# Optimization experiments

Hardware: AMD Instinct MI355X
Metric: run time of the kernel (lower is better)

The kernel has to match this reference:

```python
import jax, jax.numpy as jnp
import numpy as np

V, H, KS, VS, T, N, L = 8000, 512, 128, 128, 500, 64, 200


def setup_inputs() -> dict:
    k = jax.random.key(0)
    ks = jax.random.split(k, 16)
    s = 0.05
    emb = jax.random.normal(ks[0], (V, H), jnp.float32) * s
    emb = emb.at[0].set(0.0)  # padding_idx=0
    return {
        "key": jax.random.normal(ks[1], (T, N, KS), jnp.float32),
        "values": jax.random.normal(ks[2], (T, N, VS), jnp.float32),
        "lens": jax.random.randint(ks[3], (N,), 1, T + 1, jnp.int32),
        "text": jax.random.randint(ks[4], (N, L), 1, V, jnp.int32),
        "emb": emb,
        "W_ih1": jax.random.normal(ks[5], (4 * H, H + VS), jnp.float32) * s,
        "W_hh1": jax.random.normal(ks[6], (4 * H, H), jnp.float32) * s,
        "b_ih1": jax.random.normal(ks[7], (4 * H,), jnp.float32) * s,
        "b_hh1": jax.random.normal(ks[8], (4 * H,), jnp.float32) * s,
        "W_ih2": jax.random.normal(ks[9], (4 * KS, H), jnp.float32) * s,
        "W_hh2": jax.random.normal(ks[10], (4 * KS, KS), jnp.float32) * s,
        "b_ih2": jax.random.normal(ks[11], (4 * KS,), jnp.float32) * s,
        "b_hh2": jax.random.normal(ks[12], (4 * KS,), jnp.float32) * s,
        "W_out": jax.random.normal(ks[13], (V, KS + VS), jnp.float32) * s,
        "b_out": jax.random.normal(ks[14], (V,), jnp.float32) * s,
    }


def _lstm_cell(x, h, c, Wih, Whh, bih, bhh):
    # PyTorch LSTMCell: gates in order i, f, g, o
    z = x @ Wih.T + bih + h @ Whh.T + bhh
    i, f, g, o = jnp.split(z, 4, axis=-1)
    c2 = jax.nn.sigmoid(f) * c + jax.nn.sigmoid(i) * jnp.tanh(g)
    h2 = jax.nn.sigmoid(o) * jnp.tanh(c2)
    return h2, c2


def reference(key, values, lens, text, emb, W_ih1, W_hh1, b_ih1, b_hh1,
              W_ih2, W_hh2, b_ih2, b_hh2, W_out, b_out):
    dt = values.dtype
    # teacher-forced embeddings for all steps; padding_idx=0 -> zero vec, no grad
    embeds = emb[text] * (text != 0).astype(dt)[..., None]      # (N, L, H)
    embeds_t = jnp.swapaxes(embeds, 0, 1)                        # (L, N, H)
    key_nt = jnp.swapaxes(key, 0, 1)                             # (N, T, KS)
    val_nt = jnp.swapaxes(values, 0, 1)                          # (N, T, VS)
    pad_mask = jnp.arange(key.shape[0])[None, :] >= lens[:, None]  # (N, T)

    n = key.shape[1]
    h1 = jnp.zeros((n, W_hh1.shape[1]), dt)
    c1 = jnp.zeros_like(h1)
    h2 = jnp.zeros((n, W_hh2.shape[1]), dt)
    c2 = jnp.zeros_like(h2)
    ctx0 = values[0]  # step 0 uses values[0]; later steps use attention context

    def step(carry, char_embed):
        h1, c1, h2, c2, ctx = carry
        inp = jnp.concatenate([char_embed, ctx], axis=1)
        h1, c1 = _lstm_cell(inp, h1, c1, W_ih1, W_hh1, b_ih1, b_hh1)
        h2, c2 = _lstm_cell(h1, h2, c2, W_ih2, W_hh2, b_ih2, b_hh2)
        # attention: query = h2
        energy = jnp.einsum("ntk,nk->nt", key_nt, h2)
        energy = jnp.where(pad_mask, jnp.asarray(-1e9, dt), energy)
        attn = jax.nn.softmax(energy, axis=1)
        ctx = jnp.einsum("nt,ntv->nv", attn, val_nt)
        pred = jnp.concatenate([h2, ctx], axis=1) @ W_out.T + b_out
        return (h1, c1, h2, c2, ctx), pred

    _, preds = jax.lax.scan(step, (h1, c1, h2, c2, ctx0), embeds_t)
    return jnp.swapaxes(preds, 0, 1)  # (N, L, V)
```

## Files before the change

kernel.cpp:

```cpp
#include <hip/hip_runtime.h>
#include <hip/hip_bf16.h>


typedef __bf16 bf16;
typedef __attribute__((ext_vector_type(8))) __bf16 bf16x8;
typedef __attribute__((ext_vector_type(4))) float f32x4;
typedef unsigned int uint;

#define MFMA(a, b, c) __builtin_amdgcn_mfma_f32_16x16x32_bf16((a), (b), (c), 0, 0, 0)

#define O_X1     0UL
#define O_EMBB   52428800UL
#define O_C1     52428800UL
#define O_C2     52559872UL
#define O_WEMBP  60620800UL
#define O_WZ1    62717952UL
#define O_WZ2    65339392UL
#define O_B1P    65994752UL
#define O_B2P    66002944UL
#define O_WOUTB  66004992UL
#define O_KEYB   70100992UL
#define O_VALB   78292992UL
#define O_H1     86484992UL
#define O_H2     86616064UL
#define O_PART   86648832UL
#define O_H2CTX  86718464UL

#define AA_WA   0
#define AA_CTX  20736
#define AA_ZS   29440
#define A_LDS   46336

#define BB_WB   0
#define BB_ZS   41472
#define B_LDS   58368

#define CC_KEY  0
#define CC_VAL  33000
#define CC_EL   66000
#define CC_PL   66512
#define CC_H2F  67024
#define CC_RED  67536
#define C_LDS   67600

__device__ inline float sigf(float x) { return 1.f / (1.f + __expf(-x)); }
__device__ inline float tanhf_(float x) { float e = __expf(2.f * x); return 1.f - 2.f / (e + 1.f); }
__device__ inline float bflo(uint u) { union { uint u; float f; } c; c.u = u << 16; return c.f; }
__device__ inline float bfhi(uint u) { union { uint u; float f; } c; c.u = u & 0xffff0000u; return c.f; }
__device__ inline float wred_max(float v) {
#pragma unroll
  for (int m = 32; m; m >>= 1) v = fmaxf(v, __shfl_xor(v, m, 64));
  return v;
}
__device__ inline float wred_sum(float v) {
#pragma unroll
  for (int m = 32; m; m >>= 1) v += __shfl_xor(v, m, 64);
  return v;
}

__global__ __launch_bounds__(256) void prep_kernel(
    const float* __restrict__ key, const float* __restrict__ values,
    const float* __restrict__ emb, const float* __restrict__ Wih1,
    const float* __restrict__ Whh1, const float* __restrict__ bih1,
    const float* __restrict__ bhh1, const float* __restrict__ Wih2,
    const float* __restrict__ Whh2, const float* __restrict__ bih2,
    const float* __restrict__ bhh2, const float* __restrict__ Wout,
    char* __restrict__ ws) {
  long g = (long)blockIdx.x * 256 + threadIdx.x;
  long str = (long)gridDim.x * 256;
  bf16* embB = (bf16*)(ws + O_EMBB);
  bf16* WembP = (bf16*)(ws + O_WEMBP);
  bf16* Wz1p = (bf16*)(ws + O_WZ1);
  bf16* Wz2p = (bf16*)(ws + O_WZ2);
  float* b1p = (float*)(ws + O_B1P);
  float* b2p = (float*)(ws + O_B2P);
  bf16* WoutB = (bf16*)(ws + O_WOUTB);
  bf16* keyB = (bf16*)(ws + O_KEYB);
  bf16* valB = (bf16*)(ws + O_VALB);

  for (long i = g; i < 8000L * 512; i += str) embB[i] = (bf16)emb[i];
  for (long i = g; i < 2048L * 512; i += str) {
    long gg = i >> 9, k = i & 511;
    long pg = (gg & 3) * 512 + (gg >> 2);
    WembP[i] = (bf16)Wih1[pg * 640 + k];
  }
  for (long i = g; i < 2048L * 640; i += str) {
    long gg = i / 640, k = i - gg * 640;
    long pg = (gg & 3) * 512 + (gg >> 2);
    float v = (k < 128) ? Wih1[pg * 640 + 512 + k] : Whh1[pg * 512 + (k - 128)];
    Wz1p[i] = (bf16)v;
  }
  for (long i = g; i < 512L * 640; i += str) {
    long gg = i / 640, k = i - gg * 640;
    long pg = (gg & 3) * 128 + (gg >> 2);
    float v = (k < 128) ? Whh2[pg * 128 + k] : Wih2[pg * 512 + (k - 128)];
    Wz2p[i] = (bf16)v;
  }
  for (long i = g; i < 2048; i += str) {
    long pg = (i & 3) * 512 + (i >> 2);
    b1p[i] = bih1[pg] + bhh1[pg];
  }
  for (long i = g; i < 512; i += str) {
    long pg = (i & 3) * 128 + (i >> 2);
    b2p[i] = bih2[pg] + bhh2[pg];
  }
  for (long i = g; i < 8000L * 256; i += str) WoutB[i] = (bf16)Wout[i];
  for (long i = g; i < 500L * 64 * 128; i += str) {
    keyB[i] = (bf16)key[i];
    valB[i] = (bf16)values[i];
  }
  uint* z = (uint*)(ws + O_H1);
  for (long i = g; i < 40960; i += str) z[i] = 0u;
}

__global__ __launch_bounds__(256) void k1_gemm(const int* __restrict__ text,
                                               char* __restrict__ ws) {
  const int tid = threadIdx.x, lane = tid & 63, wave = tid >> 6;
  const int l15 = lane & 15, quad = lane >> 4;
  const int Nb = blockIdx.x, Mb = blockIdx.y;
  const bf16* embB = (const bf16*)(ws + O_EMBB);
  const bf16* WembP = (const bf16*)(ws + O_WEMBP);
  const float* b1p = (const float*)(ws + O_B1P);
  bf16* X1 = (bf16*)(ws + O_X1);

  int m = Mb * 64 + wave * 16 + l15;
  int tcol = m >> 6, n = m & 63;
  int vid = text[n * 200 + tcol];
  const bf16* arow = embB + (size_t)vid * 512 + quad * 8;

  f32x4 acc[4];
#pragma unroll
  for (int nt = 0; nt < 4; ++nt) {
    float b = b1p[Nb * 64 + nt * 16 + l15];
    acc[nt] = (f32x4){b, b, b, b};
  }
  for (int kt = 0; kt < 16; ++kt) {
    bf16x8 af = *(const bf16x8*)(arow + kt * 32);
#pragma unroll
    for (int nt = 0; nt < 4; ++nt) {
      bf16x8 bfr = *(const bf16x8*)(WembP + (size_t)(Nb * 64 + nt * 16 + l15) * 512 +
                                    kt * 32 + quad * 8);
      acc[nt] = MFMA(af, bfr, acc[nt]);
    }
  }
#pragma unroll
  for (int nt = 0; nt < 4; ++nt)
#pragma unroll
    for (int r = 0; r < 4; ++r) {
      int mr = Mb * 64 + wave * 16 + quad * 4 + r;
      X1[(size_t)mr * 2048 + Nb * 64 + nt * 16 + l15] = (bf16)acc[nt][r];
    }
}

__device__ inline void combine_ctx(int t, int nA0, int ga, int tid,
                                   bf16* __restrict__ ctx_base, const char* __restrict__ part,
                                   bf16* __restrict__ h2ctx, bool wlds) {
  int m = tid >> 3, kk = tid & 7;
  const char* pb = part + (size_t)(nA0 + m) * 4 * 272;
  float mc0 = ((const float*)(pb))[0], sc0 = ((const float*)(pb))[1];
  float mc1 = ((const float*)(pb + 272))[0], sc1 = ((const float*)(pb + 272))[1];
  float mc2 = ((const float*)(pb + 544))[0], sc2 = ((const float*)(pb + 544))[1];
  float mc3 = ((const float*)(pb + 816))[0], sc3 = ((const float*)(pb + 816))[1];
  float M = fmaxf(fmaxf(mc0, mc1), fmaxf(mc2, mc3));
  float w0 = __expf(mc0 - M), w1 = __expf(mc1 - M);
  float w2 = __expf(mc2 - M), w3 = __expf(mc3 - M);
  float S = sc0 * w0 + sc1 * w1 + sc2 * w2 + sc3 * w3;
  float inv = 1.f / S;
  const bf16* x0 = (const bf16*)(pb + 8);
  const bf16* x1 = (const bf16*)(pb + 280);
  const bf16* x2 = (const bf16*)(pb + 552);
  const bf16* x3 = (const bf16*)(pb + 824);
#pragma unroll
  for (int i = 0; i < 16; ++i) {
    int k = kk * 16 + i;
    float v = w0 * (float)x0[k] + w1 * (float)x1[k] + w2 * (float)x2[k] + w3 * (float)x3[k];
    bf16 hv = (bf16)(v * inv);
    if (wlds) ctx_base[m * 136 + k] = hv;
    if (ga == 0) h2ctx[(size_t)((t - 1) * 64 + nA0 + m) * 256 + 128 + k] = hv;
  }
}

__global__ __launch_bounds__(256) void phaseA(const float* __restrict__ values,
                                              int t, char* __restrict__ ws) {
  extern __shared__ __align__(16) char smem[];
  const int bid = blockIdx.x, tid = threadIdx.x;
  const int lane = tid & 63, wave = tid >> 6;
  const int l15 = lane & 15, quad = lane >> 4;
  const int ra = bid & 1, ga = bid >> 1;
  const int nA0 = 32 * ra;
  const int p = t & 1;

  const bf16* Wz1p = (const bf16*)(ws + O_WZ1);
  const bf16* X1 = (const bf16*)(ws + O_X1);
  bf16* h1b = (bf16*)(ws + O_H1);
  char* part = ws + O_PART;
  bf16* h2ctx = (bf16*)(ws + O_H2CTX);
  float* c1g = (float*)(ws + O_C1);

  for (int i = tid; i < 16 * 80; i += 256) {
    int r = i / 80, c = i % 80;
    *(uint4*)(smem + AA_WA + r * 1296 + c * 16) =
        *(const uint4*)((const char*)Wz1p + (size_t)(16 * ga + r) * 1280 + c * 16);
  }
  if (t == 0) {
    int m = tid >> 3, kk = tid & 7;
    bf16* ctxL = (bf16*)(smem + AA_CTX) + m * 136;
#pragma unroll
    for (int i = 0; i < 16; ++i) {
      int k = kk * 16 + i;
      ctxL[k] = (bf16)values[(nA0 + m) * 128 + k];
    }
  } else {
    combine_ctx(t, nA0, ga, tid, (bf16*)(smem + AA_CTX), part, h2ctx, true);
  }
  __syncthreads();
  {
    f32x4 acc0 = {0, 0, 0, 0}, acc1 = {0, 0, 0, 0};
    const bf16* h1p = h1b + p * 32768;
#pragma unroll
    for (int q = 0; q < 5; ++q) {
      int kt = wave * 5 + q;
      bf16x8 bfr = *(const bf16x8*)(smem + AA_WA + l15 * 1296 + (kt * 32 + quad * 8) * 2);
      bf16x8 a0, a1;
      if (kt < 4) {
        a0 = *(const bf16x8*)(smem + AA_CTX + l15 * 272 + (kt * 32 + quad * 8) * 2);
        a1 = *(const bf16x8*)(smem + AA_CTX + (16 + l15) * 272 + (kt * 32 + quad * 8) * 2);
      } else {
        const bf16* base = h1p + (kt - 4) * 32 + quad * 8;
        a0 = *(const bf16x8*)(base + (size_t)(nA0 + l15) * 512);
        a1 = *(const bf16x8*)(base + (size_t)(nA0 + 16 + l15) * 512);
      }
      acc0 = MFMA(a0, bfr, acc0);
      acc1 = MFMA(a1, bfr, acc1);
    }
    float* zs = (float*)(smem + AA_ZS) + wave * 1056;
#pragma unroll
    for (int r = 0; r < 4; ++r) {
      zs[(quad * 4 + r) * 33 + l15] = acc0[r];
      zs[(16 + quad * 4 + r) * 33 + l15] = acc1[r];
    }
  }
  __syncthreads();
  if (tid < 128) {
    int m = tid >> 2, j = tid & 3;
    float zi = 0, zf = 0, zg = 0, zo = 0;
    const float* zr = (const float*)(smem + AA_ZS);
#pragma unroll
    for (int w = 0; w < 4; ++w) {
      const float* q_ = zr + w * 1056 + m * 33 + 4 * j;
      zi += q_[0]; zf += q_[1]; zg += q_[2]; zo += q_[3];
    }
    const bf16* xp = X1 + (size_t)(t * 64 + nA0 + m) * 2048 + ga * 16 + 4 * j;
    zi += (float)xp[0]; zf += (float)xp[1]; zg += (float)xp[2]; zo += (float)xp[3];
    int ci = (nA0 + m) * 512 + ga * 4 + j;
    float cprev = (t == 0) ? 0.f : c1g[ci];
    float c = sigf(zf) * cprev + sigf(zi) * tanhf_(zg);
    float h = sigf(zo) * tanhf_(c);
    c1g[ci] = c;
    h1b[(p ^ 1) * 32768 + (size_t)(nA0 + m) * 512 + ga * 4 + j] = (bf16)h;
  }
}

__global__ __launch_bounds__(256) void phaseB(int t, char* __restrict__ ws) {
  extern __shared__ __align__(16) char smem[];
  const int bid = blockIdx.x, tid = threadIdx.x;
  const int lane = tid & 63, wave = tid >> 6;
  const int l15 = lane & 15, quad = lane >> 4;
  const int hb = bid >> 1;
  const int nB0 = 32 * (bid & 1);
  const int p = t & 1;

  const bf16* Wz2p = (const bf16*)(ws + O_WZ2);
  const float* b2p = (const float*)(ws + O_B2P);
  bf16* h1b = (bf16*)(ws + O_H1);
  bf16* h2b = (bf16*)(ws + O_H2);
  bf16* h2ctx = (bf16*)(ws + O_H2CTX);
  float* c2g = (float*)(ws + O_C2);

  for (int i = tid; i < 32 * 80; i += 256) {
    int r = i / 80, c = i % 80;
    *(uint4*)(smem + BB_WB + r * 1296 + c * 16) =
        *(const uint4*)((const char*)Wz2p + (size_t)(32 * hb + r) * 1280 + c * 16);
  }
  __syncthreads();
  {
    f32x4 a00 = {0, 0, 0, 0}, a01 = {0, 0, 0, 0}, a10 = {0, 0, 0, 0}, a11 = {0, 0, 0, 0};
    const bf16* h2p = h2b + p * 8192;
    const bf16* h1n = h1b + (p ^ 1) * 32768;
#pragma unroll
    for (int q = 0; q < 5; ++q) {
      int kt = wave * 5 + q;
      bf16x8 b0 = *(const bf16x8*)(smem + BB_WB + l15 * 1296 + (kt * 32 + quad * 8) * 2);
      bf16x8 b1 = *(const bf16x8*)(smem + BB_WB + (16 + l15) * 1296 + (kt * 32 + quad * 8) * 2);
      bf16x8 a0, a1;
      if (kt < 4) {
        const bf16* base = h2p + kt * 32 + quad * 8;
        a0 = *(const bf16x8*)(base + (size_t)(nB0 + l15) * 128);
        a1 = *(const bf16x8*)(base + (size_t)(nB0 + 16 + l15) * 128);
      } else {
        const bf16* base = h1n + (kt - 4) * 32 + quad * 8;
        a0 = *(const bf16x8*)(base + (size_t)(nB0 + l15) * 512);
        a1 = *(const bf16x8*)(base + (size_t)(nB0 + 16 + l15) * 512);
      }
      a00 = MFMA(a0, b0, a00); a01 = MFMA(a0, b1, a01);
      a10 = MFMA(a1, b0, a10); a11 = MFMA(a1, b1, a11);
    }
    float* zs = (float*)(smem + BB_ZS) + wave * 1056;
#pragma unroll
    for (int r = 0; r < 4; ++r) {
      zs[(quad * 4 + r) * 33 + l15] = a00[r];
      zs[(quad * 4 + r) * 33 + 16 + l15] = a01[r];
      zs[(16 + quad * 4 + r) * 33 + l15] = a10[r];
      zs[(16 + quad * 4 + r) * 33 + 16 + l15] = a11[r];
    }
  }
  __syncthreads();
  {
    int m = tid >> 3, jj = tid & 7;
    float zi = 0, zf = 0, zg = 0, zo = 0;
    const float* zr = (const float*)(smem + BB_ZS);
#pragma unroll
    for (int w = 0; w < 4; ++w) {
      const float* q_ = zr + w * 1056 + m * 33 + 4 * jj;
      zi += q_[0]; zf += q_[1]; zg += q_[2]; zo += q_[3];
    }
    const float* bb = b2p + 32 * hb + 4 * jj;
    zi += bb[0]; zf += bb[1]; zg += bb[2]; zo += bb[3];
    int ci = (nB0 + m) * 128 + 8 * hb + jj;
    float cprev = (t == 0) ? 0.f : c2g[ci];
    float c = sigf(zf) * cprev + sigf(zi) * tanhf_(zg);
    float h = sigf(zo) * tanhf_(c);
    c2g[ci] = c;
    bf16 hv = (bf16)h;
    h2b[(p ^ 1) * 8192 + (size_t)(nB0 + m) * 128 + 8 * hb + jj] = hv;
    h2ctx[(size_t)(t * 64 + nB0 + m) * 256 + 8 * hb + jj] = hv;
  }
}

__global__ __launch_bounds__(256) void phaseC(const int* __restrict__ lens,
                                              int t, char* __restrict__ ws) {
  extern __shared__ __align__(16) char smem[];
  const int bid = blockIdx.x, tid = threadIdx.x;
  const int lane = tid & 63, w = tid >> 6;
  const int nc = bid >> 2, cc = bid & 3;
  const int p = t & 1;

  const bf16* keyB = (const bf16*)(ws + O_KEYB);
  const bf16* valB = (const bf16*)(ws + O_VALB);
  const bf16* h2b = (const bf16*)(ws + O_H2);
  char* part = ws + O_PART;

  float* eL = (float*)(smem + CC_EL);
  float* pL = (float*)(smem + CC_PL);
  float* h2f = (float*)(smem + CC_H2F);
  float* red = (float*)(smem + CC_RED);

  for (int i = tid; i < 125 * 32; i += 256) {
    int r = i >> 5, c = i & 31;
    size_t src = ((size_t)(cc * 125 + r) * 64 + nc) * 256 + c * 8;
    *(uint2*)(smem + CC_KEY + r * 264 + c * 8) = *(const uint2*)((const char*)keyB + src);
    *(uint2*)(smem + CC_VAL + r * 264 + c * 8) = *(const uint2*)((const char*)valB + src);
  }
  if (tid < 128) h2f[tid] = (float)h2b[(p ^ 1) * 8192 + (size_t)nc * 128 + tid];
  const int lenr = lens[nc];
  __syncthreads();

  if (tid < 125) {
    int gt = cc * 125 + tid;
    float e = -1e30f;
    if (gt < lenr) {
      const uint* kr = (const uint*)(smem + CC_KEY + tid * 264);
      float s = 0.f;
#pragma unroll 8
      for (int k2 = 0; k2 < 64; ++k2) {
        uint u = kr[k2];
        s += h2f[2 * k2] * bflo(u) + h2f[2 * k2 + 1] * bfhi(u);
      }
      e = s;
    }
    eL[tid] = e;
  } else if (tid < 128) {
    eL[tid] = -1e30f;
  }
  __syncthreads();
  if (tid < 64) {
    float v = fmaxf(eL[tid], eL[tid + 64]);
    v = wred_max(v);
    if (tid == 0) red[0] = v;
  }
  __syncthreads();
  float mC = red[0];
  if (tid < 128) {
    float pv = 0.f;
    if (tid < 125 && (cc * 125 + tid) < lenr) pv = __expf(eL[tid] - mC);
    pL[tid] = pv;
  }
  __syncthreads();
  if (tid < 64) {
    float v = pL[tid] + pL[tid + 64];
    v = wred_sum(v);
    if (tid == 0) red[1] = v;
  }
  __syncthreads();
  {
    char* pbase = part + (size_t)(nc * 4 + cc) * 272;
    if (tid == 0) {
      ((float*)pbase)[0] = mC;
      ((float*)pbase)[1] = red[1];
    }
    if (tid < 64) {
      const char* vbase = smem + CC_VAL + tid * 4;
      float a0 = 0.f, a1 = 0.f;
      for (int tt = 0; tt < 125; ++tt) {
        float pv = pL[tt];
        uint u = *(const uint*)(vbase + tt * 264);
        a0 += pv * bflo(u);
        a1 += pv * bfhi(u);
      }
      bf16* dst = (bf16*)(pbase + 8);
      dst[2 * tid] = (bf16)a0;
      dst[2 * tid + 1] = (bf16)a1;
    }
  }
}

__global__ __launch_bounds__(256) void ctx_final(char* __restrict__ ws) {
  const int nA0 = 32 * blockIdx.x, tid = threadIdx.x;
  combine_ctx(200, nA0, 0, tid, nullptr, ws + O_PART, (bf16*)(ws + O_H2CTX), false);
}

__global__ __launch_bounds__(256) void k4_gemm(const float* __restrict__ bout,
                                               float* __restrict__ out,
                                               char* __restrict__ ws) {
  const int tid = threadIdx.x, lane = tid & 63, wave = tid >> 6;
  const int l15 = lane & 15, quad = lane >> 4;
  const int Nb = blockIdx.x, Mb = blockIdx.y;
  const bf16* A = (const bf16*)(ws + O_H2CTX);
  const bf16* B = (const bf16*)(ws + O_WOUTB);

  int mrow = Mb * 64 + wave * 16 + l15;
  const bf16* arow = A + (size_t)mrow * 256 + quad * 8;

  int vs[8];
  f32x4 acc[8];
#pragma unroll
  for (int nt = 0; nt < 8; ++nt) {
    int v = Nb * 128 + nt * 16 + l15;
    vs[nt] = v < 8000 ? v : 7999;
    float b = (v < 8000) ? bout[v] : 0.f;
    acc[nt] = (f32x4){b, b, b, b};
  }
#pragma unroll
  for (int kt = 0; kt < 8; ++kt) {
    bf16x8 af = *(const bf16x8*)(arow + kt * 32);
#pragma unroll
    for (int nt = 0; nt < 8; ++nt) {
      bf16x8 bfr = *(const bf16x8*)(B + (size_t)vs[nt] * 256 + kt * 32 + quad * 8);
      acc[nt] = MFMA(af, bfr, acc[nt]);
    }
  }
#pragma unroll
  for (int nt = 0; nt < 8; ++nt) {
    int v = Nb * 128 + nt * 16 + l15;
    if (v < 8000) {
#pragma unroll
      for (int r = 0; r < 4; ++r) {
        int mr = Mb * 64 + wave * 16 + quad * 4 + r;
        int n = mr & 63, tt = mr >> 6;
        out[(size_t)(n * 200 + tt) * 8000 + v] = acc[nt][r];
      }
    }
  }
}

extern "C" void kernel_launch(void* const* d_in, const int* in_sizes, int n_in,
                              void* d_out, int out_size, void* d_ws, size_t ws_size,
                              hipStream_t stream) {
  const float* key = (const float*)d_in[0];
  const float* values = (const float*)d_in[1];
  const int* lens = (const int*)d_in[2];
  const int* text = (const int*)d_in[3];
  const float* emb = (const float*)d_in[4];
  const float* Wih1 = (const float*)d_in[5];
  const float* Whh1 = (const float*)d_in[6];
  const float* bih1 = (const float*)d_in[7];
  const float* bhh1 = (const float*)d_in[8];
  const float* Wih2 = (const float*)d_in[9];
  const float* Whh2 = (const float*)d_in[10];
  const float* bih2 = (const float*)d_in[11];
  const float* bhh2 = (const float*)d_in[12];
  const float* Wout = (const float*)d_in[13];
  const float* bout = (const float*)d_in[14];
  float* out = (float*)d_out;
  char* ws = (char*)d_ws;

  hipFuncSetAttribute(reinterpret_cast<const void*>(phaseC),
                      hipFuncAttributeMaxDynamicSharedMemorySize, 160 * 1024);

  prep_kernel<<<1024, 256, 0, stream>>>(key, values, emb, Wih1, Whh1, bih1, bhh1,
                                        Wih2, Whh2, bih2, bhh2, Wout, ws);
  k1_gemm<<<dim3(32, 200), 256, 0, stream>>>(text, ws);
  for (int t = 0; t < 200; ++t) {
    phaseA<<<256, 256, A_LDS, stream>>>(values, t, ws);
    phaseB<<<32, 256, B_LDS, stream>>>(t, ws);
    phaseC<<<256, 256, C_LDS, stream>>>(lens, t, ws);
  }
  ctx_final<<<2, 256, 0, stream>>>(ws);
  k4_gemm<<<dim3(63, 200), 256, 0, stream>>>(bout, out, ws);
}
```

Before: 6.220 ms.

## Fuse second LSTM cell into attention kernel with redundant per-block computation

Merges phaseB (second LSTM cell) into phaseC (attention), so each of the 256 attention blocks recomputes the layer-2 gates for its own batch row using MFMA against Wz2 streamed from global memory. Only the cc==0 block writes c2/h2 state, and c2 becomes double-buffered to avoid read/write races between blocks. This removes one kernel launch and a global round-trip per timestep, out of 200 steps. In exchange it does 4x redundant layer-2 gate work and has every block read the full Wz2 from global/L2, which also adds latency to each step.

```diff
diff --git a/kernel.cpp b/kernel.cpp
--- a/kernel.cpp
+++ b/kernel.cpp
@@ -31,17 +31,15 @@
 #define AA_ZS   29440
 #define A_LDS   46336
 
-#define BB_WB   0
-#define BB_ZS   41472
-#define B_LDS   58368
-
-#define CC_KEY  0
-#define CC_VAL  33000
-#define CC_EL   66000
-#define CC_PL   66512
-#define CC_H2F  67024
-#define CC_RED  67536
-#define C_LDS   67600
+#define BC_KEY  0
+#define BC_VAL  33000
+#define BC_X2   66000
+#define BC_ZL   67280
+#define BC_H2F  69328
+#define BC_EL   69840
+#define BC_PL   70352
+#define BC_RED  70864
+#define BC_LDS  70928
 
 __device__ inline float sigf(float x) { return 1.f / (1.f + __expf(-x)); }
 __device__ inline float tanhf_(float x) { float e = __expf(2.f * x); return 1.f - 2.f / (e + 1.f); }
@@ -261,115 +259,87 @@
   }
 }
 
-__global__ __launch_bounds__(256) void phaseB(int t, char* __restrict__ ws) {
+__global__ __launch_bounds__(256, 1) void phaseBC(const int* __restrict__ lens,
+                                                  int t, char* __restrict__ ws) {
   extern __shared__ __align__(16) char smem[];
   const int bid = blockIdx.x, tid = threadIdx.x;
-  const int lane = tid & 63, wave = tid >> 6;
+  const int lane = tid & 63, w = tid >> 6;
   const int l15 = lane & 15, quad = lane >> 4;
-  const int hb = bid >> 1;
-  const int nB0 = 32 * (bid & 1);
+  const int nc = bid >> 2, cc = bid & 3;
   const int p = t & 1;
 
+  const bf16* keyB = (const bf16*)(ws + O_KEYB);
+  const bf16* valB = (const bf16*)(ws + O_VALB);
   const bf16* Wz2p = (const bf16*)(ws + O_WZ2);
   const float* b2p = (const float*)(ws + O_B2P);
-  bf16* h1b = (bf16*)(ws + O_H1);
+  const bf16* h1b = (const bf16*)(ws + O_H1);
   bf16* h2b = (bf16*)(ws + O_H2);
   bf16* h2ctx = (bf16*)(ws + O_H2CTX);
   float* c2g = (float*)(ws + O_C2);
-
-  for (int i = tid; i < 32 * 80; i += 256) {
-    int r = i / 80, c = i % 80;
-    *(uint4*)(smem + BB_WB + r * 1296 + c * 16) =
-        *(const uint4*)((const char*)Wz2p + (size_t)(32 * hb + r) * 1280 + c * 16);
-  }
-  __syncthreads();
-  {
-    f32x4 a00 = {0, 0, 0, 0}, a01 = {0, 0, 0, 0}, a10 = {0, 0, 0, 0}, a11 = {0, 0, 0, 0};
-    const bf16* h2p = h2b + p * 8192;
-    const bf16* h1n = h1b + (p ^ 1) * 32768;
-#pragma unroll
-    for (int q = 0; q < 5; ++q) {
-      int kt = wave * 5 + q;
-      bf16x8 b0 = *(const bf16x8*)(smem + BB_WB + l15 * 1296 + (kt * 32 + quad * 8) * 2);
-      bf16x8 b1 = *(const bf16x8*)(smem + BB_WB + (16 + l15) * 1296 + (kt * 32 + quad * 8) * 2);
-      bf16x8 a0, a1;
-      if (kt < 4) {
-        const bf16* base = h2p + kt * 32 + quad * 8;
-        a0 = *(const bf16x8*)(base + (size_t)(nB0 + l15) * 128);
-        a1 = *(const bf16x8*)(base + (size_t)(nB0 + 16 + l15) * 128);
-      } else {
-        const bf16* base = h1n + (kt - 4) * 32 + quad * 8;
-        a0 = *(const bf16x8*)(base + (size_t)(nB0 + l15) * 512);
-        a1 = *(const bf16x8*)(base + (size_t)(nB0 + 16 + l15) * 512);
-      }
-      a00 = MFMA(a0, b0, a00); a01 = MFMA(a0, b1, a01);
-      a10 = MFMA(a1, b0, a10); a11 = MFMA(a1, b1, a11);
-    }
-    float* zs = (float*)(smem + BB_ZS) + wave * 1056;
-#pragma unroll
-    for (int r = 0; r < 4; ++r) {
-      zs[(quad * 4 + r) * 33 + l15] = a00[r];
-      zs[(quad * 4 + r) * 33 + 16 + l15] = a01[r];
-      zs[(16 + quad * 4 + r) * 33 + l15] = a10[r];
-      zs[(16 + quad * 4 + r) * 33 + 16 + l15] = a11[r];
-    }
-  }
-  __syncthreads();
-  {
-    int m = tid >> 3, jj = tid & 7;
-    float zi = 0, zf = 0, zg = 0, zo = 0;
-    const float* zr = (const float*)(smem + BB_ZS);
-#pragma unroll
-    for (int w = 0; w < 4; ++w) {
-      const float* q_ = zr + w * 1056 + m * 33 + 4 * jj;
-      zi += q_[0]; zf += q_[1]; zg += q_[2]; zo += q_[3];
-    }
-    const float* bb = b2p + 32 * hb + 4 * jj;
-    zi += bb[0]; zf += bb[1]; zg += bb[2]; zo += bb[3];
-    int ci = (nB0 + m) * 128 + 8 * hb + jj;
-    float cprev = (t == 0) ? 0.f : c2g[ci];
-    float c = sigf(zf) * cprev + sigf(zi) * tanhf_(zg);
-    float h = sigf(zo) * tanhf_(c);
-    c2g[ci] = c;
-    bf16 hv = (bf16)h;
-    h2b[(p ^ 1) * 8192 + (size_t)(nB0 + m) * 128 + 8 * hb + jj] = hv;
-    h2ctx[(size_t)(t * 64 + nB0 + m) * 256 + 8 * hb + jj] = hv;
-  }
-}
-
-__global__ __launch_bounds__(256) void phaseC(const int* __restrict__ lens,
-                                              int t, char* __restrict__ ws) {
-  extern __shared__ __align__(16) char smem[];
-  const int bid = blockIdx.x, tid = threadIdx.x;
-  const int lane = tid & 63, w = tid >> 6;
-  const int nc = bid >> 2, cc = bid & 3;
-  const int p = t & 1;
-
-  const bf16* keyB = (const bf16*)(ws + O_KEYB);
-  const bf16* valB = (const bf16*)(ws + O_VALB);
-  const bf16* h2b = (const bf16*)(ws + O_H2);
   char* part = ws + O_PART;
 
-  float* eL = (float*)(smem + CC_EL);
-  float* pL = (float*)(smem + CC_PL);
-  float* h2f = (float*)(smem + CC_H2F);
-  float* red = (float*)(smem + CC_RED);
+  bf16* x2L = (bf16*)(smem + BC_X2);
+  float* zL = (float*)(smem + BC_ZL);
+  float* h2f = (float*)(smem + BC_H2F);
+  float* eL = (float*)(smem + BC_EL);
+  float* pL = (float*)(smem + BC_PL);
+  float* red = (float*)(smem + BC_RED);
 
   for (int i = tid; i < 125 * 32; i += 256) {
     int r = i >> 5, c = i & 31;
     size_t src = ((size_t)(cc * 125 + r) * 64 + nc) * 256 + c * 8;
-    *(uint2*)(smem + CC_KEY + r * 264 + c * 8) = *(const uint2*)((const char*)keyB + src);
-    *(uint2*)(smem + CC_VAL + r * 264 + c * 8) = *(const uint2*)((const char*)valB + src);
-  }
-  if (tid < 128) h2f[tid] = (float)h2b[(p ^ 1) * 8192 + (size_t)nc * 128 + tid];
+    *(uint2*)(smem + BC_KEY + r * 264 + c * 8) = *(const uint2*)((const char*)keyB + src);
+    *(uint2*)(smem + BC_VAL + r * 264 + c * 8) = *(const uint2*)((const char*)valB + src);
+  }
+  if (tid < 128) x2L[tid] = h2b[p * 8192 + nc * 128 + tid];
+  x2L[128 + tid] = h1b[(p ^ 1) * 32768 + nc * 512 + tid];
+  x2L[384 + tid] = h1b[(p ^ 1) * 32768 + nc * 512 + 256 + tid];
   const int lenr = lens[nc];
   __syncthreads();
 
+  {
+    bf16x8 af[20];
+#pragma unroll
+    for (int kt = 0; kt < 20; ++kt)
+      af[kt] = *(const bf16x8*)(smem + BC_X2 + kt * 64 + quad * 16);
+    for (int tp = 0; tp < 4; ++tp) {
+      int g0 = (w * 8 + tp * 2) * 16 + l15;
+      const bf16* B0 = Wz2p + (size_t)g0 * 640 + quad * 8;
+      const bf16* B1 = B0 + 16 * 640;
+      f32x4 a0 = {0.f, 0.f, 0.f, 0.f}, a1 = {0.f, 0.f, 0.f, 0.f};
+#pragma unroll
+      for (int kt = 0; kt < 20; ++kt) {
+        a0 = MFMA(af[kt], *(const bf16x8*)(B0 + kt * 32), a0);
+        a1 = MFMA(af[kt], *(const bf16x8*)(B1 + kt * 32), a1);
+      }
+      if (quad == 0) {
+        zL[g0] = a0[0];
+        zL[g0 + 16] = a1[0];
+      }
+    }
+  }
+  __syncthreads();
+  if (tid < 128) {
+    float4 zv = *(const float4*)(zL + 4 * tid);
+    float4 bb = *(const float4*)(b2p + 4 * tid);
+    float zi = zv.x + bb.x, zf = zv.y + bb.y, zg = zv.z + bb.z, zo = zv.w + bb.w;
+    float cprev = (t == 0) ? 0.f : c2g[p * 8192 + nc * 128 + tid];
+    float c = sigf(zf) * cprev + sigf(zi) * tanhf_(zg);
+    float h = sigf(zo) * tanhf_(c);
+    h2f[tid] = h;
+    if (cc == 0) {
+      c2g[(p ^ 1) * 8192 + nc * 128 + tid] = c;
+      bf16 hv = (bf16)h;
+      h2b[(p ^ 1) * 8192 + nc * 128 + tid] = hv;
+      h2ctx[(size_t)(t * 64 + nc) * 256 + tid] = hv;
+    }
+  }
+  __syncthreads();
   if (tid < 125) {
     int gt = cc * 125 + tid;
     float e = -1e30f;
     if (gt < lenr) {
-      const uint* kr = (const uint*)(smem + CC_KEY + tid * 264);
+      const uint* kr = (const uint*)(smem + BC_KEY + tid * 264);
       float s = 0.f;
 #pragma unroll 8
       for (int k2 = 0; k2 < 64; ++k2) {
@@ -409,7 +379,7 @@
       ((float*)pbase)[1] = red[1];
     }
     if (tid < 64) {
-      const char* vbase = smem + CC_VAL + tid * 4;
+      const char* vbase = smem + BC_VAL + tid * 4;
       float a0 = 0.f, a1 = 0.f;
       for (int tt = 0; tt < 125; ++tt) {
         float pv = pL[tt];
@@ -494,7 +464,7 @@
   float* out = (float*)d_out;
   char* ws = (char*)d_ws;
 
-  hipFuncSetAttribute(reinterpret_cast<const void*>(phaseC),
+  hipFuncSetAttribute(reinterpret_cast<const void*>(phaseBC),
                       hipFuncAttributeMaxDynamicSharedMemorySize, 160 * 1024);
 
   prep_kernel<<<1024, 256, 0, stream>>>(key, values, emb, Wih1, Whh1, bih1, bhh1,
@@ -502,8 +472,7 @@
   k1_gemm<<<dim3(32, 200), 256, 0, stream>>>(text, ws);
   for (int t = 0; t < 200; ++t) {
     phaseA<<<256, 256, A_LDS, stream>>>(values, t, ws);
-    phaseB<<<32, 256, B_LDS, stream>>>(t, ws);
-    phaseC<<<256, 256, C_LDS, stream>>>(lens, t, ws);
+    phaseBC<<<256, 256, BC_LDS, stream>>>(lens, t, ws);
   }
   ctx_final<<<2, 256, 0, stream>>>(ws);
   k4_gemm<<<dim3(63, 200), 256, 0, stream>>>(bout, out, ws);
```

Measured after the change: 8.876 ms. +42.7%, slower.
